# Kernel optimization log

Measured on AMD Instinct MI355X. Metric: run time of the kernel, lower is better.

## Reference

```python
import jax, jax.numpy as jnp
import numpy as np

N = 6144
IN_F = 512
OUT_F = 64
NHEADS = 8
ALPHA = 0.2  # leaky_relu negative slope
NEG_BIG = -1e10


def setup_inputs() -> dict:
    key = jax.random.key(0)
    k1, k2, k3, k4, k5 = jax.random.split(key, 5)
    x = jax.random.normal(k1, (N, IN_F), dtype=jnp.float32)
    adj = (jax.random.uniform(k2, (N, N)) < 0.01).astype(jnp.float32)
    adj = jnp.maximum(adj, jnp.eye(N, dtype=jnp.float32))
    weight = jax.random.normal(k3, (IN_F, NHEADS * OUT_F), dtype=jnp.float32) * 0.05
    linear_i = jax.random.normal(k4, (1, NHEADS, OUT_F), dtype=jnp.float32) * 0.05
    linear_j = jax.random.normal(k5, (1, NHEADS, OUT_F), dtype=jnp.float32) * 0.05
    return {"x": x, "adj": adj, "weight": weight, "linear_i": linear_i, "linear_j": linear_j}


def reference(x, adj, weight, linear_i, linear_j):
    # dropout p=0.0 (inference) -> identity
    wh = (x @ weight).reshape(-1, NHEADS, OUT_F)          # [N, H, F]
    awh_i = jnp.sum(wh * linear_i, axis=2)[:, None, :]    # [N, 1, H]
    awh_j = jnp.sum(wh * linear_j, axis=2)[None, :, :]    # [1, N, H]
    mask = (NEG_BIG * (1.0 - adj))[:, :, None]            # [N, N, 1]
    e = jax.nn.leaky_relu(awh_i + awh_j, negative_slope=ALPHA) + mask  # [N, N, H]
    a = jax.nn.softmax(e, axis=1)                          # softmax over source nodes j
    out = jnp.einsum('ijh,jhf->ihf', a, wh)               # [N, H, F]
    return out.reshape(out.shape[0], -1)                  # concat heads -> [N, H*F]
```

## Files before the change

### kernel.cpp

```cpp
#include <hip/hip_runtime.h>
#include <math.h>

#define N_NODES 6144
#define IN_FEAT 512
#define OUTW    512
#define NH      8
#define ALPHA   0.2f
#define CAP     128
#define GEMM_BLKS 768
#define CSR_BLKS  1536

typedef __attribute__((ext_vector_type(8))) short short8;
typedef __attribute__((ext_vector_type(4))) float f32x4;

__device__ __forceinline__ unsigned short f2bf(float f) {
    unsigned int u = __float_as_uint(f);
    u = (u + 0x7fffu + ((u >> 16) & 1u)) >> 16;
    return (unsigned short)u;
}
__device__ __forceinline__ float bf2f(unsigned short b) {
    return __uint_as_float(((unsigned int)b) << 16);
}

__global__ __launch_bounds__(256) void conv_w(const float* __restrict__ W,
                                              unsigned short* __restrict__ WThi,
                                              unsigned short* __restrict__ WTlo) {
    int n  = blockIdx.x * 8 + (threadIdx.x >> 5);
    int k0 = (threadIdx.x & 31) * 16;
    union { unsigned short u[16]; uint4 q[2]; } th, tl;
#pragma unroll
    for (int kk = 0; kk < 16; ++kk) {
        float v = W[(size_t)(k0 + kk) * OUTW + n];
        unsigned short hi = f2bf(v);
        th.u[kk] = hi;
        tl.u[kk] = f2bf(v - bf2f(hi));
    }
    uint4* ph = (uint4*)(WThi + (size_t)n * IN_FEAT + k0);
    uint4* pl = (uint4*)(WTlo + (size_t)n * IN_FEAT + k0);
    ph[0] = th.q[0]; ph[1] = th.q[1];
    pl[0] = tl.q[0]; pl[1] = tl.q[1];
}

__global__ __launch_bounds__(256) void gemm_csr(const float* __restrict__ X,
                                                const unsigned short* __restrict__ BThi,
                                                const unsigned short* __restrict__ BTlo,
                                                const float* __restrict__ LI,
                                                const float* __restrict__ LJ,
                                                const float* __restrict__ ADJ,
                                                unsigned short* __restrict__ WHB,
                                                float* __restrict__ AI,
                                                float* __restrict__ AJ,
                                                int* __restrict__ NBR,
                                                int* __restrict__ CNT) {
    __shared__ unsigned short As[64][40];
    __shared__ unsigned short Bh[64][40];
    __shared__ unsigned short Bl[64][40];
    __shared__ float s_ap[64][2], s_jp[64][2];
    const int tid = threadIdx.x;
    const int wave = tid >> 6, lane = tid & 63;

    if (blockIdx.x >= GEMM_BLKS) {
        const int row = (blockIdx.x - GEMM_BLKS) * 4 + wave;
        const f32x4* r4 = (const f32x4*)(ADJ + (size_t)row * N_NODES);
        int* dst = NBR + (size_t)row * CAP;
        const unsigned long long lt = (1ULL << lane) - 1;
        int base = 0;
#pragma unroll
        for (int q = 0; q < 24; ++q) {
            f32x4 v = __builtin_nontemporal_load(r4 + q * 64 + lane);
            int j = (q * 64 + lane) * 4;
#pragma unroll
            for (int c = 0; c < 4; ++c) {
                bool pred = v[c] > 0.5f;
                unsigned long long m = __ballot(pred);
                if (pred) {
                    int p = base + __popcll(m & lt);
                    if (p < CAP) dst[p] = j + c;
                }
                base += __popcll(m);
            }
        }
        if (lane == 0) CNT[row] = min(base, CAP);
        return;
    }

    const int bn = (blockIdx.x & 7) * 64, bm = (blockIdx.x >> 3) * 64;
    const int head = blockIdx.x & 7;
    const int wm0 = (wave & 1) * 32, wn0 = (wave >> 1) * 32;
    const int lm = lane & 15, lg = lane >> 4;
    const int ar = tid >> 2, akq = (tid & 3) * 8;
    f32x4 acc[2][2] = {};
    for (int k0 = 0; k0 < IN_FEAT; k0 += 32) {
        const float* ap = X + (size_t)(bm + ar) * IN_FEAT + k0 + akq;
        float4 f0 = *(const float4*)ap;
        float4 f1 = *(const float4*)(ap + 4);
        union { unsigned short u[8]; uint4 q; } ah;
        ah.u[0] = f2bf(f0.x); ah.u[1] = f2bf(f0.y);
        ah.u[2] = f2bf(f0.z); ah.u[3] = f2bf(f0.w);
        ah.u[4] = f2bf(f1.x); ah.u[5] = f2bf(f1.y);
        ah.u[6] = f2bf(f1.z); ah.u[7] = f2bf(f1.w);
        *(uint4*)&As[ar][akq] = ah.q;
        *(uint4*)&Bh[ar][akq] = *(const uint4*)(BThi + (size_t)(bn + ar) * IN_FEAT + k0 + akq);
        *(uint4*)&Bl[ar][akq] = *(const uint4*)(BTlo + (size_t)(bn + ar) * IN_FEAT + k0 + akq);
        __syncthreads();
        short8 a0  = *(const short8*)&As[wm0 + lm][lg * 8];
        short8 a1  = *(const short8*)&As[wm0 + 16 + lm][lg * 8];
        short8 bh0 = *(const short8*)&Bh[wn0 + lm][lg * 8];
        short8 bh1 = *(const short8*)&Bh[wn0 + 16 + lm][lg * 8];
        short8 bl0 = *(const short8*)&Bl[wn0 + lm][lg * 8];
        short8 bl1 = *(const short8*)&Bl[wn0 + 16 + lm][lg * 8];
        acc[0][0] = __builtin_amdgcn_mfma_f32_16x16x32_bf16(a0, bh0, acc[0][0], 0, 0, 0);
        acc[0][0] = __builtin_amdgcn_mfma_f32_16x16x32_bf16(a0, bl0, acc[0][0], 0, 0, 0);
        acc[0][1] = __builtin_amdgcn_mfma_f32_16x16x32_bf16(a0, bh1, acc[0][1], 0, 0, 0);
        acc[0][1] = __builtin_amdgcn_mfma_f32_16x16x32_bf16(a0, bl1, acc[0][1], 0, 0, 0);
        acc[1][0] = __builtin_amdgcn_mfma_f32_16x16x32_bf16(a1, bh0, acc[1][0], 0, 0, 0);
        acc[1][0] = __builtin_amdgcn_mfma_f32_16x16x32_bf16(a1, bl0, acc[1][0], 0, 0, 0);
        acc[1][1] = __builtin_amdgcn_mfma_f32_16x16x32_bf16(a1, bh1, acc[1][1], 0, 0, 0);
        acc[1][1] = __builtin_amdgcn_mfma_f32_16x16x32_bf16(a1, bl1, acc[1][1], 0, 0, 0);
        __syncthreads();
    }
#pragma unroll
    for (int fm = 0; fm < 2; ++fm)
#pragma unroll
        for (int fn = 0; fn < 2; ++fn)
#pragma unroll
            for (int r = 0; r < 4; ++r) {
                int row = bm + wm0 + fm * 16 + lg * 4 + r;
                int col = bn + wn0 + fn * 16 + lm;
                WHB[(size_t)row * OUTW + col] = f2bf(acc[fm][fn][r]);
            }
    float liv0 = LI[bn + wn0 + lm], liv1 = LI[bn + wn0 + 16 + lm];
    float ljv0 = LJ[bn + wn0 + lm], ljv1 = LJ[bn + wn0 + 16 + lm];
#pragma unroll
    for (int fm = 0; fm < 2; ++fm)
#pragma unroll
        for (int r = 0; r < 4; ++r) {
            float pa = acc[fm][0][r] * liv0 + acc[fm][1][r] * liv1;
            float pj = acc[fm][0][r] * ljv0 + acc[fm][1][r] * ljv1;
#pragma unroll
            for (int off = 1; off < 16; off <<= 1) {
                pa += __shfl_xor(pa, off);
                pj += __shfl_xor(pj, off);
            }
            if (lm == 0) {
                int row = wm0 + fm * 16 + lg * 4 + r;
                s_ap[row][wave >> 1] = pa;
                s_jp[row][wave >> 1] = pj;
            }
        }
    __syncthreads();
    if (tid < 64) {
        AI[(size_t)(bm + tid) * NH + head] = s_ap[tid][0] + s_ap[tid][1];
        AJ[(size_t)(bm + tid) * NH + head] = s_jp[tid][0] + s_jp[tid][1];
    }
}

__global__ __launch_bounds__(256) void gat_attn(const unsigned short* __restrict__ WHB,
                                                const float* __restrict__ AI,
                                                const float* __restrict__ AJ,
                                                const int* __restrict__ NBR,
                                                const int* __restrict__ CNT,
                                                float* __restrict__ OUT) {
    __shared__ int   s_nbr[CAP];
    __shared__ float s_p[CAP][9];
    __shared__ float s_comb[4][512];
    __shared__ float s_ai[8];
    __shared__ float s_red[4][8];
    __shared__ float s_m[8];
    __shared__ float s_d[8];

    const int i   = blockIdx.x;
    const int tid = threadIdx.x;
    const int wid = tid >> 6, lane = tid & 63;
    const int nc  = min(CNT[i], CAP);

    if (tid < 8) s_ai[tid] = AI[i * 8 + tid];
    if (tid < nc) s_nbr[tid] = NBR[(size_t)i * CAP + tid];
    __syncthreads();

    float mx[8];
#pragma unroll
    for (int h = 0; h < 8; ++h) mx[h] = -1e30f;
    if (tid < nc) {
        int j = s_nbr[tid];
        const float* ajp = AJ + (size_t)j * 8;
        float4 a0 = *(const float4*)ajp;
        float4 a1 = *(const float4*)(ajp + 4);
        float z[8] = {a0.x, a0.y, a0.z, a0.w, a1.x, a1.y, a1.z, a1.w};
#pragma unroll
        for (int h = 0; h < 8; ++h) {
            float zz = s_ai[h] + z[h];
            float s  = zz > 0.f ? zz : ALPHA * zz;
            s_p[tid][h] = s;
            mx[h] = fmaxf(mx[h], s);
        }
    }
#pragma unroll
    for (int off = 32; off > 0; off >>= 1)
#pragma unroll
        for (int h = 0; h < 8; ++h) mx[h] = fmaxf(mx[h], __shfl_down(mx[h], off));
    if (lane == 0)
#pragma unroll
        for (int h = 0; h < 8; ++h) s_red[wid][h] = mx[h];
    __syncthreads();
    if (tid < 8)
        s_m[tid] = fmaxf(fmaxf(s_red[0][tid], s_red[1][tid]),
                         fmaxf(s_red[2][tid], s_red[3][tid]));
    __syncthreads();

    float sm[8] = {0.f, 0.f, 0.f, 0.f, 0.f, 0.f, 0.f, 0.f};
    if (tid < nc) {
#pragma unroll
        for (int h = 0; h < 8; ++h) {
            float p = __expf(s_p[tid][h] - s_m[h]);
            s_p[tid][h] = p;
            sm[h] += p;
        }
    }
#pragma unroll
    for (int off = 32; off > 0; off >>= 1)
#pragma unroll
        for (int h = 0; h < 8; ++h) sm[h] += __shfl_down(sm[h], off);
    if (lane == 0)
#pragma unroll
        for (int h = 0; h < 8; ++h) s_red[wid][h] = sm[h];
    __syncthreads();
    if (tid < 8)
        s_d[tid] = s_red[0][tid] + s_red[1][tid] + s_red[2][tid] + s_red[3][tid];
    __syncthreads();

    const int hd = lane >> 3;
    float a8[8] = {};
    uint4 p0 = {}, p1 = {};
    const int k0 = wid;
    if (k0 < nc)     p0 = *(const uint4*)(WHB + (size_t)s_nbr[k0] * OUTW + lane * 8);
    if (k0 + 4 < nc) p1 = *(const uint4*)(WHB + (size_t)s_nbr[k0 + 4] * OUTW + lane * 8);
    for (int k = k0; k < nc; k += 4) {
        uint4 curw = p0;
        p0 = p1;
        if (k + 8 < nc) p1 = *(const uint4*)(WHB + (size_t)s_nbr[k + 8] * OUTW + lane * 8);
        float p = s_p[k][hd];
        unsigned int uu[4] = {curw.x, curw.y, curw.z, curw.w};
#pragma unroll
        for (int q = 0; q < 4; ++q) {
            float lo = __uint_as_float(uu[q] << 16);
            float hi = __uint_as_float(uu[q] & 0xFFFF0000u);
            a8[2 * q]     += p * lo;
            a8[2 * q + 1] += p * hi;
        }
    }
#pragma unroll
    for (int q = 0; q < 8; ++q) s_comb[wid][lane * 8 + q] = a8[q];
    __syncthreads();
    if (tid < 128) {
        int c0 = tid * 4;
        int hh = tid >> 4;
        float4 v0 = *(const float4*)&s_comb[0][c0];
        float4 v1 = *(const float4*)&s_comb[1][c0];
        float4 v2 = *(const float4*)&s_comb[2][c0];
        float4 v3 = *(const float4*)&s_comb[3][c0];
        float inv = 1.0f / s_d[hh];
        float4 res;
        res.x = (v0.x + v1.x + v2.x + v3.x) * inv;
        res.y = (v0.y + v1.y + v2.y + v3.y) * inv;
        res.z = (v0.z + v1.z + v2.z + v3.z) * inv;
        res.w = (v0.w + v1.w + v2.w + v3.w) * inv;
        *(float4*)(OUT + (size_t)i * OUTW + c0) = res;
    }
}

extern "C" void kernel_launch(void* const* d_in, const int* in_sizes, int n_in,
                              void* d_out, int out_size, void* d_ws, size_t ws_size,
                              hipStream_t stream) {
    const float* x   = (const float*)d_in[0];
    const float* adj = (const float*)d_in[1];
    const float* w   = (const float*)d_in[2];
    const float* li  = (const float*)d_in[3];
    const float* lj  = (const float*)d_in[4];
    float* out = (float*)d_out;

    unsigned short* whb = (unsigned short*)d_ws;
    float* ai = (float*)(whb + (size_t)N_NODES * OUTW);
    float* aj = ai + (size_t)N_NODES * NH;
    unsigned short* wthi = (unsigned short*)(aj + (size_t)N_NODES * NH);
    unsigned short* wtlo = wthi + (size_t)OUTW * IN_FEAT;
    int* nbr = (int*)(wtlo + (size_t)OUTW * IN_FEAT);
    int* cnt = nbr + (size_t)N_NODES * CAP;

    conv_w<<<OUTW / 8, 256, 0, stream>>>(w, wthi, wtlo);
    gemm_csr<<<GEMM_BLKS + CSR_BLKS, 256, 0, stream>>>(
        x, wthi, wtlo, li, lj, adj, whb, ai, aj, nbr, cnt);
    gat_attn<<<N_NODES, 256, 0, stream>>>(whb, ai, aj, nbr, cnt, out);
}
```

Baseline: 106.3 us.

## Drop bf16 split-weight correction and interleave GEMM with CSR build blocks

Removes the low-order bf16 residual of the weights, so the projection GEMM does half the MFMAs and loads one B tile instead of two. Block indices are remapped so every GEMM block is followed by two adjacency-compaction blocks, mixing compute-bound and bandwidth-bound work across the GPU rather than running them in sequence. The output store becomes a nontemporal store. Weight precision drops to plain bf16, which adds error to wh and the attention logits.

```diff
diff --git a/kernel.cpp b/kernel.cpp
--- a/kernel.cpp
+++ b/kernel.cpp
@@ -7,8 +7,7 @@
 #define NH      8
 #define ALPHA   0.2f
 #define CAP     128
-#define GEMM_BLKS 768
-#define CSR_BLKS  1536
+#define TOTAL_BLKS 2304
 
 typedef __attribute__((ext_vector_type(8))) short short8;
 typedef __attribute__((ext_vector_type(4))) float f32x4;
@@ -18,32 +17,21 @@
     u = (u + 0x7fffu + ((u >> 16) & 1u)) >> 16;
     return (unsigned short)u;
 }
-__device__ __forceinline__ float bf2f(unsigned short b) {
-    return __uint_as_float(((unsigned int)b) << 16);
-}
 
 __global__ __launch_bounds__(256) void conv_w(const float* __restrict__ W,
-                                              unsigned short* __restrict__ WThi,
-                                              unsigned short* __restrict__ WTlo) {
+                                              unsigned short* __restrict__ WThi) {
     int n  = blockIdx.x * 8 + (threadIdx.x >> 5);
     int k0 = (threadIdx.x & 31) * 16;
-    union { unsigned short u[16]; uint4 q[2]; } th, tl;
-#pragma unroll
-    for (int kk = 0; kk < 16; ++kk) {
-        float v = W[(size_t)(k0 + kk) * OUTW + n];
-        unsigned short hi = f2bf(v);
-        th.u[kk] = hi;
-        tl.u[kk] = f2bf(v - bf2f(hi));
-    }
+    union { unsigned short u[16]; uint4 q[2]; } th;
+#pragma unroll
+    for (int kk = 0; kk < 16; ++kk)
+        th.u[kk] = f2bf(W[(size_t)(k0 + kk) * OUTW + n]);
     uint4* ph = (uint4*)(WThi + (size_t)n * IN_FEAT + k0);
-    uint4* pl = (uint4*)(WTlo + (size_t)n * IN_FEAT + k0);
     ph[0] = th.q[0]; ph[1] = th.q[1];
-    pl[0] = tl.q[0]; pl[1] = tl.q[1];
 }
 
 __global__ __launch_bounds__(256) void gemm_csr(const float* __restrict__ X,
                                                 const unsigned short* __restrict__ BThi,
-                                                const unsigned short* __restrict__ BTlo,
                                                 const float* __restrict__ LI,
                                                 const float* __restrict__ LJ,
                                                 const float* __restrict__ ADJ,
@@ -54,13 +42,14 @@
                                                 int* __restrict__ CNT) {
     __shared__ unsigned short As[64][40];
     __shared__ unsigned short Bh[64][40];
-    __shared__ unsigned short Bl[64][40];
     __shared__ float s_ap[64][2], s_jp[64][2];
     const int tid = threadIdx.x;
     const int wave = tid >> 6, lane = tid & 63;
-
-    if (blockIdx.x >= GEMM_BLKS) {
-        const int row = (blockIdx.x - GEMM_BLKS) * 4 + wave;
+    const int bid = blockIdx.x;
+    const int g = bid / 3, r3 = bid - g * 3;
+
+    if (r3 != 0) {
+        const int row = (g * 2 + (r3 - 1)) * 4 + wave;
         const f32x4* r4 = (const f32x4*)(ADJ + (size_t)row * N_NODES);
         int* dst = NBR + (size_t)row * CAP;
         const unsigned long long lt = (1ULL << lane) - 1;
@@ -84,8 +73,8 @@
         return;
     }
 
-    const int bn = (blockIdx.x & 7) * 64, bm = (blockIdx.x >> 3) * 64;
-    const int head = blockIdx.x & 7;
+    const int bn = (g & 7) * 64, bm = (g >> 3) * 64;
+    const int head = g & 7;
     const int wm0 = (wave & 1) * 32, wn0 = (wave >> 1) * 32;
     const int lm = lane & 15, lg = lane >> 4;
     const int ar = tid >> 2, akq = (tid & 3) * 8;
@@ -101,22 +90,15 @@
         ah.u[6] = f2bf(f1.z); ah.u[7] = f2bf(f1.w);
         *(uint4*)&As[ar][akq] = ah.q;
         *(uint4*)&Bh[ar][akq] = *(const uint4*)(BThi + (size_t)(bn + ar) * IN_FEAT + k0 + akq);
-        *(uint4*)&Bl[ar][akq] = *(const uint4*)(BTlo + (size_t)(bn + ar) * IN_FEAT + k0 + akq);
         __syncthreads();
         short8 a0  = *(const short8*)&As[wm0 + lm][lg * 8];
         short8 a1  = *(const short8*)&As[wm0 + 16 + lm][lg * 8];
         short8 bh0 = *(const short8*)&Bh[wn0 + lm][lg * 8];
         short8 bh1 = *(const short8*)&Bh[wn0 + 16 + lm][lg * 8];
-        short8 bl0 = *(const short8*)&Bl[wn0 + lm][lg * 8];
-        short8 bl1 = *(const short8*)&Bl[wn0 + 16 + lm][lg * 8];
         acc[0][0] = __builtin_amdgcn_mfma_f32_16x16x32_bf16(a0, bh0, acc[0][0], 0, 0, 0);
-        acc[0][0] = __builtin_amdgcn_mfma_f32_16x16x32_bf16(a0, bl0, acc[0][0], 0, 0, 0);
         acc[0][1] = __builtin_amdgcn_mfma_f32_16x16x32_bf16(a0, bh1, acc[0][1], 0, 0, 0);
-        acc[0][1] = __builtin_amdgcn_mfma_f32_16x16x32_bf16(a0, bl1, acc[0][1], 0, 0, 0);
         acc[1][0] = __builtin_amdgcn_mfma_f32_16x16x32_bf16(a1, bh0, acc[1][0], 0, 0, 0);
-        acc[1][0] = __builtin_amdgcn_mfma_f32_16x16x32_bf16(a1, bl0, acc[1][0], 0, 0, 0);
         acc[1][1] = __builtin_amdgcn_mfma_f32_16x16x32_bf16(a1, bh1, acc[1][1], 0, 0, 0);
-        acc[1][1] = __builtin_amdgcn_mfma_f32_16x16x32_bf16(a1, bl1, acc[1][1], 0, 0, 0);
         __syncthreads();
     }
 #pragma unroll
@@ -260,12 +242,12 @@
         float4 v2 = *(const float4*)&s_comb[2][c0];
         float4 v3 = *(const float4*)&s_comb[3][c0];
         float inv = 1.0f / s_d[hh];
-        float4 res;
+        f32x4 res;
         res.x = (v0.x + v1.x + v2.x + v3.x) * inv;
         res.y = (v0.y + v1.y + v2.y + v3.y) * inv;
         res.z = (v0.z + v1.z + v2.z + v3.z) * inv;
         res.w = (v0.w + v1.w + v2.w + v3.w) * inv;
-        *(float4*)(OUT + (size_t)i * OUTW + c0) = res;
+        __builtin_nontemporal_store(res, (f32x4*)(OUT + (size_t)i * OUTW + c0));
     }
 }
 
@@ -283,12 +265,11 @@
     float* ai = (float*)(whb + (size_t)N_NODES * OUTW);
     float* aj = ai + (size_t)N_NODES * NH;
     unsigned short* wthi = (unsigned short*)(aj + (size_t)N_NODES * NH);
-    unsigned short* wtlo = wthi + (size_t)OUTW * IN_FEAT;
-    int* nbr = (int*)(wtlo + (size_t)OUTW * IN_FEAT);
+    int* nbr = (int*)(wthi + (size_t)OUTW * IN_FEAT);
     int* cnt = nbr + (size_t)N_NODES * CAP;
 
-    conv_w<<<OUTW / 8, 256, 0, stream>>>(w, wthi, wtlo);
-    gemm_csr<<<GEMM_BLKS + CSR_BLKS, 256, 0, stream>>>(
-        x, wthi, wtlo, li, lj, adj, whb, ai, aj, nbr, cnt);
+    conv_w<<<OUTW / 8, 256, 0, stream>>>(w, wthi);
+    gemm_csr<<<TOTAL_BLKS, 256, 0, stream>>>(
+        x, wthi, li, lj, adj, whb, ai, aj, nbr, cnt);
     gat_attn<<<N_NODES, 256, 0, stream>>>(whb, ai, aj, nbr, cnt, out);
 }
```

Measured after the change: 101.0 us. 4.9% less time.
